# Kernel optimization log

Measured on AMD Instinct MI355X. Metric: run time of the kernel, lower is better.

The kernel has to match this reference:

```python
import jax, jax.numpy as jnp
import numpy as np

DIM = 512
HID = 1024        # dim * expansion_factor
QK = 128          # query_key_dim
G = 256           # group_size
EPS = 1e-5


def setup_inputs() -> dict:
    key = jax.random.key(0)
    ks = jax.random.split(key, 6)
    x = jax.random.normal(ks[0], (4, 4096, DIM), jnp.float32)
    ln_w = jnp.ones((DIM,), jnp.float32)
    ln_b = jnp.zeros((DIM,), jnp.float32)
    Wh = 0.02 * jax.random.normal(ks[1], (DIM, 2 * HID), jnp.float32)
    bh = jnp.zeros((2 * HID,), jnp.float32)
    Wqk = 0.02 * jax.random.normal(ks[2], (DIM, QK), jnp.float32)
    bqk = jnp.zeros((QK,), jnp.float32)
    gamma = 0.02 * jax.random.normal(ks[3], (4, QK), jnp.float32)  # nn.init.normal_(gamma, std=0.02)
    beta = jnp.zeros((4, QK), jnp.float32)
    Wo = 0.02 * jax.random.normal(ks[4], (HID, DIM), jnp.float32)
    bo = jnp.zeros((DIM,), jnp.float32)
    return {"x": x, "ln_w": ln_w, "ln_b": ln_b, "Wh": Wh, "bh": bh,
            "Wqk": Wqk, "bqk": bqk, "gamma": gamma, "beta": beta,
            "Wo": Wo, "bo": bo}


def reference(x, ln_w, ln_b, Wh, bh, Wqk, bqk, gamma, beta, Wo, bo):
    b, n, _ = x.shape
    g = n // G  # number of groups (n chosen as multiple of G -> no padding)

    # LayerNorm (torch uses biased variance)
    mu = jnp.mean(x, axis=-1, keepdims=True)
    var = jnp.mean((x - mu) ** 2, axis=-1, keepdims=True)
    normed = (x - mu) * jax.lax.rsqrt(var + EPS) * ln_w + ln_b

    # to_hidden: Linear -> SiLU, split into v / gate
    h = jax.nn.silu(normed @ Wh + bh)            # [b, n, 2*HID]
    v, gate = jnp.split(h, 2, axis=-1)           # each [b, n, HID]

    # to_qk: Linear -> SiLU, then 4-head offset/scale
    qk = jax.nn.silu(normed @ Wqk + bqk)         # [b, n, QK]
    qkh = qk[..., None, :] * gamma + beta        # [b, n, 4, QK]
    quad_q, lin_q, quad_k, lin_k = (qkh[..., i, :] for i in range(4))

    # group: b (g n) d -> b g n d
    grp = lambda t: t.reshape(b, g, G, t.shape[-1])
    qq, qk_, lq, lk, vv = map(grp, (quad_q, quad_k, lin_q, lin_k, v))

    # quadratic (group-local) attention with ReLU^2 scores, causal within group
    sim = jnp.einsum('bgid,bgjd->bgij', qq, qk_) / G
    attn = jnp.square(jnp.maximum(sim, 0.0))
    causal_mask = jnp.triu(jnp.ones((G, G), dtype=bool), 1)
    attn = jnp.where(causal_mask, 0.0, attn)
    quad_out = jnp.einsum('bgij,bgje->bgie', attn, vv)   # [b, g, G, HID]

    # linear attention across groups: per-group kv, exclusive cumsum over group dim
    lin_kv = jnp.einsum('bgnd,bgne->bgde', lk, vv) / G   # [b, g, QK, HID]
    lin_kv = jnp.cumsum(lin_kv, axis=1)
    lin_kv = jnp.pad(lin_kv, ((0, 0), (1, 0), (0, 0), (0, 0)))[:, :-1]
    lin_out = jnp.einsum('bgde,bgnd->bgne', lin_kv, lq)  # [b, g, G, HID]

    out = gate * (quad_out.reshape(b, n, HID) + lin_out.reshape(b, n, HID))
    return out @ Wo + bo + x
```

## Files before the change

kernel.cpp:

```cpp
#include <hip/hip_runtime.h>
#include <hip/hip_bf16.h>
#include <math.h>


#define BATCH 4
#define SEQ   4096
#define TROWS 16384
#define DIMD  512
#define HIDD  1024
#define QKD   128
#define GRP   256
#define NGRP  16
#define BGRP  64
#define EPIW  132
#define EPB   130

typedef unsigned short bfraw;
typedef __attribute__((ext_vector_type(8))) short bf16x8;
typedef __attribute__((ext_vector_type(8))) unsigned short u16x8;
typedef __attribute__((ext_vector_type(4))) unsigned int u32x4;
typedef __attribute__((ext_vector_type(4))) float f32x4;

__device__ __forceinline__ float bf2f(bfraw u) {
    union { float f; unsigned int i; } c;
    c.i = ((unsigned int)u) << 16;
    return c.f;
}
__device__ __forceinline__ bfraw f2bf(float f) {
    unsigned int x = __float_as_uint(f);
    unsigned int r = (x + 0x7fffu + ((x >> 16) & 1u)) >> 16;
    return (bfraw)r;
}
__device__ __forceinline__ unsigned int pkbf(float lo, float hi) {
    __hip_bfloat162 h2 = __float22bfloat162_rn(make_float2(lo, hi));
    union { __hip_bfloat162 h; unsigned int u; } c; c.h = h2;
    return c.u;
}
__device__ __forceinline__ void store16bf(bfraw* dst, const float* src) {
    u32x4 a, b;
    #pragma unroll
    for (int k = 0; k < 4; ++k) a[k] = pkbf(src[2 * k], src[2 * k + 1]);
    #pragma unroll
    for (int k = 0; k < 4; ++k) b[k] = pkbf(src[8 + 2 * k], src[8 + 2 * k + 1]);
    *(u32x4*)dst = a;
    *(u32x4*)(dst + 8) = b;
}
__device__ __forceinline__ float silu_f(float z) {
    return z / (1.f + __expf(-z));
}
__device__ __forceinline__ void gload_lds16(const void* g, void* l) {
    __builtin_amdgcn_global_load_lds(
        (const __attribute__((address_space(1))) unsigned int*)g,
        (__attribute__((address_space(3))) unsigned int*)l, 16, 0, 0);
}

__device__ __forceinline__ void mfma_step(const bfraw* As, const bfraw* Bs,
                                          f32x4 acc[4][4], int wm, int wn,
                                          int q, int mi) {
    bf16x8 af[4], bfg[4];
    #pragma unroll
    for (int i = 0; i < 4; ++i)
        af[i] = *(const bf16x8*)&As[(size_t)(wm * 64 + i * 16 + mi) * 32 + q * 8];
    #pragma unroll
    for (int j = 0; j < 4; ++j)
        bfg[j] = *(const bf16x8*)&Bs[(size_t)(wn * 64 + j * 16 + mi) * 32 + q * 8];
    #pragma unroll
    for (int i = 0; i < 4; ++i)
        #pragma unroll
        for (int j = 0; j < 4; ++j)
            acc[i][j] = __builtin_amdgcn_mfma_f32_16x16x32_bf16(af[i], bfg[j], acc[i][j], 0, 0, 0);
}

#define SMEMP_DECL                                              \
    __shared__ __align__(16) char smem_[33280];                 \
    bfraw* A0buf = (bfraw*)smem_;                               \
    bfraw* B0buf = (bfraw*)(smem_ + 8192);                      \
    bfraw* A1buf = (bfraw*)(smem_ + 16384);                     \
    bfraw* B1buf = (bfraw*)(smem_ + 24576);

#define PIPE_DSTS                                               \
    bfraw* a0d  = A0buf + wid * 512;                            \
    bfraw* a0d2 = A0buf + 2048 + wid * 512;                     \
    bfraw* b0d  = B0buf + wid * 512;                            \
    bfraw* b0d2 = B0buf + 2048 + wid * 512;                     \
    bfraw* a1d  = A1buf + wid * 512;                            \
    bfraw* a1d2 = A1buf + 2048 + wid * 512;                     \
    bfraw* b1d  = B1buf + wid * 512;                            \
    bfraw* b1d2 = B1buf + 2048 + wid * 512;

#define KLOOP_PRE(Abase, Astr, Bbase, Bstr)                                    \
    const bfraw* pa0 = (Abase) + (size_t)(t >> 2) * (Astr) + (t & 3) * 8;      \
    const bfraw* pa1 = pa0 + (size_t)64 * (Astr);                              \
    const bfraw* pb0 = (Bbase) + (size_t)(t >> 2) * (Bstr) + (t & 3) * 8;      \
    const bfraw* pb1 = pb0 + (size_t)64 * (Bstr);

#define STAGE0                                                                 \
    do { gload_lds16(pa0, a0d); gload_lds16(pa1, a0d2);                        \
         gload_lds16(pb0, b0d); gload_lds16(pb1, b0d2);                        \
         pa0 += 32; pa1 += 32; pb0 += 32; pb1 += 32; } while (0)
#define STAGE1                                                                 \
    do { gload_lds16(pa0, a1d); gload_lds16(pa1, a1d2);                        \
         gload_lds16(pb0, b1d); gload_lds16(pb1, b1d2);                        \
         pa0 += 32; pa1 += 32; pb0 += 32; pb1 += 32; } while (0)

#define PIPE_LOOP(NIT, Abase, Astr, Bbase, Bstr)                               \
    {                                                                          \
        KLOOP_PRE(Abase, Astr, Bbase, Bstr)                                    \
        STAGE0;                                                                \
        for (int it = 0; it < (NIT); it += 2) {                                \
            __syncthreads();                                                   \
            if (it + 1 < (NIT)) STAGE1;                                        \
            mfma_step(A0buf, B0buf, acc, wm, wn, q, mi);                       \
            __syncthreads();                                                   \
            if (it + 2 < (NIT)) STAGE0;                                        \
            if (it + 1 < (NIT))                                                \
                mfma_step(A1buf, B1buf, acc, wm, wn, q, mi);                   \
        }                                                                      \
        __syncthreads();                                                       \
    }

__device__ __forceinline__ int epi_row(int p, int lr) {
    return (lr < 16) ? (p * 16 + lr) : (64 + p * 16 + (lr - 16));
}

__global__ __launch_bounds__(256) void prep_kernel(const float* __restrict__ x,
                                                   const float* __restrict__ lnw,
                                                   const float* __restrict__ lnb,
                                                   const float* __restrict__ Wh,
                                                   const float* __restrict__ Wo,
                                                   const float* __restrict__ Wqk,
                                                   bfraw* __restrict__ normb,
                                                   bfraw* __restrict__ WhT,
                                                   bfraw* __restrict__ WoT,
                                                   bfraw* __restrict__ WqkT) {
    __shared__ float tile[32][33];
    int bid = blockIdx.x;
    int t = threadIdx.x;
    if (bid < 4096) {
        int row  = bid * 4 + (t >> 6);
        int lane = t & 63;
        const float* xr = x + (size_t)row * DIMD;
        float4 v0 = ((const float4*)xr)[lane];
        float4 v1 = ((const float4*)xr)[lane + 64];
        float s  = v0.x + v0.y + v0.z + v0.w + v1.x + v1.y + v1.z + v1.w;
        float ss = v0.x*v0.x + v0.y*v0.y + v0.z*v0.z + v0.w*v0.w
                 + v1.x*v1.x + v1.y*v1.y + v1.z*v1.z + v1.w*v1.w;
        #pragma unroll
        for (int off = 32; off; off >>= 1) {
            s  += __shfl_xor(s, off);
            ss += __shfl_xor(ss, off);
        }
        float mu  = s * (1.f / DIMD);
        float var = ss * (1.f / DIMD) - mu * mu;
        float inv = rsqrtf(var + 1e-5f);
        float4 w0 = ((const float4*)lnw)[lane],  w1 = ((const float4*)lnw)[lane + 64];
        float4 b0 = ((const float4*)lnb)[lane],  b1 = ((const float4*)lnb)[lane + 64];
        unsigned int o0 = pkbf((v0.x - mu) * inv * w0.x + b0.x,
                               (v0.y - mu) * inv * w0.y + b0.y);
        unsigned int o1 = pkbf((v0.z - mu) * inv * w0.z + b0.z,
                               (v0.w - mu) * inv * w0.w + b0.w);
        unsigned int o2 = pkbf((v1.x - mu) * inv * w1.x + b1.x,
                               (v1.y - mu) * inv * w1.y + b1.y);
        unsigned int o3 = pkbf((v1.z - mu) * inv * w1.z + b1.z,
                               (v1.w - mu) * inv * w1.w + b1.w);
        unsigned int* brow = (unsigned int*)(normb + (size_t)row * DIMD);
        ((uint2*)brow)[lane]      = make_uint2(o0, o1);
        ((uint2*)brow)[lane + 64] = make_uint2(o2, o3);
        return;
    }
    bid -= 4096;
    const float* in; bfraw* outp; int R, C, nx;
    if (bid < 1024)      { in = Wh;  outp = WhT;  R = DIMD; C = 2 * HIDD; nx = 64; }
    else if (bid < 1536) { bid -= 1024; in = Wo;  outp = WoT;  R = HIDD; C = DIMD; nx = 16; }
    else                 { bid -= 1536; in = Wqk; outp = WqkT; R = DIMD; C = QKD;  nx = 4; }
    int c0 = (bid % nx) * 32, r0 = (bid / nx) * 32;
    int tr = t >> 3, tc4 = (t & 7) * 4;
    float4 v = *(const float4*)&in[(size_t)(r0 + tr) * C + c0 + tc4];
    tile[tr][tc4 + 0] = v.x; tile[tr][tc4 + 1] = v.y;
    tile[tr][tc4 + 2] = v.z; tile[tr][tc4 + 3] = v.w;
    __syncthreads();
    ushort4 s;
    s.x = f2bf(tile[tc4 + 0][tr]);
    s.y = f2bf(tile[tc4 + 1][tr]);
    s.z = f2bf(tile[tc4 + 2][tr]);
    s.w = f2bf(tile[tc4 + 3][tr]);
    *(ushort4*)&outp[(size_t)(c0 + tr) * R + r0 + tc4] = s;
}

__global__ __launch_bounds__(1024, 4) void gemm_h256(
    const bfraw* __restrict__ A,
    const bfraw* __restrict__ WhT,
    const bfraw* __restrict__ WqkT,
    const float* __restrict__ bh,
    const float* __restrict__ bqk,
    const float* __restrict__ gamma,
    const float* __restrict__ beta,
    bfraw* __restrict__ vT,
    bfraw* __restrict__ gate,
    bfraw* __restrict__ qq,
    bfraw* __restrict__ lq,
    bfraw* __restrict__ kk,
    bfraw* __restrict__ lkT) {
    __shared__ __align__(16) char smem_[131072];
    const int t = threadIdx.x;
    const int lane = t & 63, wid = t >> 6;
    const int wm = wid >> 2, wn = wid & 3;
    const int q = lane >> 4, mi = lane & 15;
    int nid = (blockIdx.x & 7) * 72 + (blockIdx.x >> 3);
    const int ct = nid % 9, by = nid / 9;
    const int r0 = by * 256, c0 = ct * 256;

    const int lslot = (t & 7) ^ ((t >> 3) & 7);
    const int srow  = 2 * (t >> 3) + (lslot >> 2);
    const int skel  = (lslot & 3) * 8;
    const bfraw* Asrc = A + (size_t)(r0 + srow) * DIMD + skel;
    const bfraw* Bsrc;
    if (ct < 8) {
        Bsrc = WhT + (size_t)(c0 + srow) * DIMD + skel;
    } else {
        Bsrc = WqkT + (size_t)(srow & 127) * DIMD + skel;
    }
    const int swz = ((((mi & 1) << 2) | q) ^ ((mi >> 1) & 7)) << 4;
    const int a_off = (wm * 32 + (mi >> 1)) * 128 + swz;
    const int b_off = (wn * 32 + (mi >> 1)) * 128 + swz;

#define GH_STAGE(KT, SLOT)                                                    \
    do {                                                                      \
        char* sb_ = smem_ + (SLOT) * 32768;                                   \
        gload_lds16(Asrc + (KT) * 32, sb_ + t * 16);                          \
        gload_lds16(Bsrc + (KT) * 32, sb_ + 16384 + t * 16);                  \
    } while (0)

    f32x4 acc[4][4] = {};
    GH_STAGE(0, 0);
    GH_STAGE(1, 1);
    GH_STAGE(2, 2);
    asm volatile("s_waitcnt vmcnt(4)" ::: "memory");
    __builtin_amdgcn_s_barrier();

    #pragma unroll
    for (int j = 0; j < 16; ++j) {
        const char* cb = smem_ + (j & 3) * 32768;
        bf16x8 af[4], bfr[4];
        #pragma unroll
        for (int mf = 0; mf < 4; ++mf)
            af[mf] = *(const bf16x8*)(cb + a_off + mf * 1024);
        #pragma unroll
        for (int nf = 0; nf < 4; ++nf)
            bfr[nf] = *(const bf16x8*)(cb + 16384 + b_off + nf * 1024);
        if (j + 3 < 16) GH_STAGE(j + 3, (j + 3) & 3);
        __builtin_amdgcn_s_setprio(1);
        #pragma unroll
        for (int mf = 0; mf < 4; ++mf)
            #pragma unroll
            for (int nf = 0; nf < 4; ++nf)
                acc[mf][nf] = __builtin_amdgcn_mfma_f32_16x16x32_bf16(
                    af[mf], bfr[nf], acc[mf][nf], 0, 0, 0);
        __builtin_amdgcn_s_setprio(0);
        if (j + 3 < 16)      asm volatile("s_waitcnt vmcnt(4)" ::: "memory");
        else if (j + 2 < 16) asm volatile("s_waitcnt vmcnt(2)" ::: "memory");
        else if (j + 1 < 16) asm volatile("s_waitcnt vmcnt(0)" ::: "memory");
        __builtin_amdgcn_s_barrier();
    }
#undef GH_STAGE

    float* epi = (float*)smem_;
    if (ct == 8) {
        float* gbl = (float*)(smem_ + 67584);
        if (t < 512) { gbl[t] = gamma[t]; gbl[t + 512] = beta[t]; }
        float bq4[4];
        #pragma unroll
        for (int nf = 0; nf < 4; ++nf)
            bq4[nf] = (wn < 2) ? bqk[wn * 64 + nf * 16 + mi] : 0.f;
        #pragma unroll
        for (int p = 0; p < 4; ++p) {
            if (wm == p && wn < 2) {
                #pragma unroll
                for (int mf = 0; mf < 4; ++mf)
                    #pragma unroll
                    for (int nf = 0; nf < 4; ++nf)
                        #pragma unroll
                        for (int rg = 0; rg < 4; ++rg)
                            epi[(mf * 16 + q * 4 + rg) * 132 + wn * 64 + nf * 16 + mi] =
                                silu_f(acc[mf][nf][rg] + bq4[nf]);
            }
            __syncthreads();
            if (t < 512) {
                int lr = t >> 3, cs = (t & 7) * 16;
                float z[16];
                #pragma unroll
                for (int k = 0; k < 16; ++k) z[k] = epi[lr * 132 + cs + k];
                size_t growr = (size_t)(r0 + p * 64 + lr) * QKD + cs;
                #pragma unroll
                for (int hd = 0; hd < 3; ++hd) {
                    bfraw* arr = (hd == 0) ? qq : (hd == 1) ? lq : kk;
                    float tmp[16];
                    #pragma unroll
                    for (int k = 0; k < 16; ++k)
                        tmp[k] = z[k] * gbl[hd * 128 + cs + k] + gbl[512 + hd * 128 + cs + k];
                    store16bf(arr + growr, tmp);
                }
            } else {
                int tt = t - 512;
                int c = tt >> 2, jh = (tt & 3) * 16;
                float g3 = gbl[384 + c], e3 = gbl[896 + c];
                float tmp[16];
                #pragma unroll
                for (int k = 0; k < 16; ++k)
                    tmp[k] = epi[(jh + k) * 132 + c] * g3 + e3;
                store16bf(lkT + ((size_t)by * QKD + c) * GRP + p * 64 + jh, tmp);
            }
            __syncthreads();
        }
        return;
    }
    float bias4[4];
    #pragma unroll
    for (int nf = 0; nf < 4; ++nf)
        bias4[nf] = bh[c0 + wn * 64 + nf * 16 + mi];
    if (ct < 4) {
        #pragma unroll
        for (int p = 0; p < 4; ++p) {
            if (wm == p) {
                #pragma unroll
                for (int mf = 0; mf < 4; ++mf)
                    #pragma unroll
                    for (int nf = 0; nf < 4; ++nf)
                        #pragma unroll
                        for (int rg = 0; rg < 4; ++rg)
                            epi[(mf * 16 + q * 4 + rg) * 257 + wn * 64 + nf * 16 + mi] =
                                silu_f(acc[mf][nf][rg] + bias4[nf]);
            }
            __syncthreads();
            int e2 = t >> 2, js = (t & 3) * 16;
            float tmp[16];
            #pragma unroll
            for (int k = 0; k < 16; ++k)
                tmp[k] = epi[(js + k) * 257 + e2];
            store16bf(vT + ((size_t)by * HIDD + c0 + e2) * GRP + p * 64 + js, tmp);
            __syncthreads();
        }
    } else {
        #pragma unroll
        for (int p = 0; p < 4; ++p) {
            if (wm == p) {
                #pragma unroll
                for (int mf = 0; mf < 4; ++mf)
                    #pragma unroll
                    for (int nf = 0; nf < 4; ++nf)
                        #pragma unroll
                        for (int rg = 0; rg < 4; ++rg)
                            epi[(mf * 16 + q * 4 + rg) * 260 + wn * 64 + nf * 16 + mi] =
                                silu_f(acc[mf][nf][rg] + bias4[nf]);
            }
            __syncthreads();
            int lr = t >> 4, cs = (t & 15) * 16;
            float tmp[16];
            #pragma unroll
            for (int k = 0; k < 16; ++k)
                tmp[k] = epi[lr * 260 + cs + k];
            store16bf(gate + (size_t)(r0 + p * 64 + lr) * HIDD + (c0 - HIDD) + cs, tmp);
            __syncthreads();
        }
    }
}

__global__ __launch_bounds__(256) void simkv_kernel(const bfraw* __restrict__ qq,
                                                    const bfraw* __restrict__ kk,
                                                    bfraw* __restrict__ attn,
                                                    const bfraw* __restrict__ vT,
                                                    const bfraw* __restrict__ lkT,
                                                    bfraw* __restrict__ kvT_raw) {
    SMEMP_DECL
    float* epi = (float*)smem_;
    int t = threadIdx.x;
    int lane = t & 63, wid = t >> 6;
    int wm = wid >> 1, wn = wid & 1;
    int q = lane >> 4, mi = lane & 15;
    int bid = blockIdx.x;
    f32x4 acc[4][4] = {};
    PIPE_DSTS
    if (bid < 512) {
        int bg = bid >> 3;
        int row0 = (bid & 7) * 128;
        PIPE_LOOP(8, vT + (size_t)bg * HIDD * GRP + (size_t)row0 * GRP, GRP,
                  lkT + (size_t)bg * QKD * GRP, GRP)
        bfraw* outg = kvT_raw + (size_t)bg * HIDD * QKD;
        #pragma unroll
        for (int p = 0; p < 4; ++p) {
            #pragma unroll
            for (int j = 0; j < 4; ++j)
                #pragma unroll
                for (int rg = 0; rg < 4; ++rg)
                    epi[(wm * 16 + q * 4 + rg) * EPIW + wn * 64 + j * 16 + mi] = acc[p][j][rg];
            __syncthreads();
            int lr = t >> 3, c0t = (t & 7) * 16;
            int gr = row0 + epi_row(p, lr);
            store16bf(outg + (size_t)gr * QKD + c0t, &epi[lr * EPIW + c0t]);
            __syncthreads();
        }
        return;
    }
    int i = bid - 512;
    int bg = i & 63;
    int tid = i >> 6;
    int ry = (tid == 0) ? 0 : 1;
    int rx = (tid == 2) ? 1 : 0;
    int row0 = ry * 128, col0 = rx * 128;
    PIPE_LOOP(4, qq + (size_t)(bg * GRP + row0) * QKD, QKD,
              kk + (size_t)(bg * GRP + col0) * QKD, QKD)
    bfraw* ag = attn + (size_t)bg * GRP * GRP;
    #pragma unroll
    for (int p = 0; p < 4; ++p) {
        #pragma unroll
        for (int j = 0; j < 4; ++j) {
            int colg = col0 + wn * 64 + j * 16 + mi;
            #pragma unroll
            for (int rg = 0; rg < 4; ++rg) {
                int rowg = row0 + wm * 64 + p * 16 + q * 4 + rg;
                float s = acc[p][j][rg] * (1.f / GRP);
                s = fmaxf(s, 0.f);
                s = s * s;
                epi[(wm * 16 + q * 4 + rg) * EPIW + wn * 64 + j * 16 + mi] =
                    (colg > rowg) ? 0.f : s;
            }
        }
        __syncthreads();
        int lr = t >> 3, c0t = (t & 7) * 16;
        int gr = row0 + epi_row(p, lr);
        store16bf(ag + (size_t)gr * GRP + col0 + c0t, &epi[lr * EPIW + c0t]);
        __syncthreads();
    }
}

__global__ __launch_bounds__(256) void cumsum2_kernel(const bfraw* __restrict__ raw,
                                                      bfraw* __restrict__ ex) {
    int idx = blockIdx.x * 256 + threadIdx.x;
    int b = idx >> 17;
    int r = idx & 131071;
    const bfraw* rp = raw + (size_t)b * NGRP * 131072 + r;
    bfraw* ep = ex + (size_t)b * NGRP * 131072 + r;
    float run = 0.f;
    #pragma unroll
    for (int g = 0; g < NGRP; ++g) {
        ep[(size_t)g * 131072] = f2bf(run);
        run += bf2f(rp[(size_t)g * 131072]) * (1.f / GRP);
    }
}

__global__ __launch_bounds__(256) void quadlin_mfma(const bfraw* __restrict__ attn,
                                                    const bfraw* __restrict__ vT,
                                                    const bfraw* __restrict__ lq,
                                                    const bfraw* __restrict__ kvT_ex,
                                                    const bfraw* __restrict__ gate,
                                                    bfraw* __restrict__ gated) {
    int bg = blockIdx.z;
    int row0 = blockIdx.y * 128;
    int col0 = blockIdx.x * 128;
    SMEMP_DECL
    float* epi = (float*)smem_;
    int t = threadIdx.x;
    int lane = t & 63, wid = t >> 6;
    int wm = wid >> 1, wn = wid & 1;
    int q = lane >> 4, mi = lane & 15;
    f32x4 acc[4][4] = {};
    PIPE_DSTS
    {
        int nit = (row0 + 128) >> 5;
        PIPE_LOOP(nit, attn + (size_t)bg * GRP * GRP + (size_t)row0 * GRP, GRP,
                  vT + (size_t)bg * HIDD * GRP + (size_t)col0 * GRP, GRP)
    }
    PIPE_LOOP(4, lq + (size_t)(bg * GRP + row0) * QKD, QKD,
              kvT_ex + (size_t)bg * HIDD * QKD + (size_t)col0 * QKD, QKD)
    #pragma unroll
    for (int p = 0; p < 4; ++p) {
        #pragma unroll
        for (int j = 0; j < 4; ++j)
            #pragma unroll
            for (int rg = 0; rg < 4; ++rg)
                epi[(wm * 16 + q * 4 + rg) * EPIW + wn * 64 + j * 16 + mi] = acc[p][j][rg];
        __syncthreads();
        int lr = t >> 3, c0t = (t & 7) * 16;
        int gr = row0 + epi_row(p, lr);
        size_t grow = (size_t)bg * GRP + gr;
        const float* src = &epi[lr * EPIW + c0t];
        const bfraw* gsrc = gate + grow * HIDD + col0 + c0t;
        u16x8 g0 = *(const u16x8*)gsrc;
        u16x8 g1 = *(const u16x8*)(gsrc + 8);
        float tmp[16];
        #pragma unroll
        for (int k = 0; k < 8; ++k) tmp[k] = src[k] * bf2f(g0[k]);
        #pragma unroll
        for (int k = 0; k < 8; ++k) tmp[8 + k] = src[8 + k] * bf2f(g1[k]);
        store16bf(gated + grow * HIDD + col0 + c0t, tmp);
        __syncthreads();
    }
}

__global__ __launch_bounds__(256) void gemm_final(const bfraw* __restrict__ A,
                                                  const bfraw* __restrict__ BT,
                                                  const float* __restrict__ bo,
                                                  const float* __restrict__ x,
                                                  float* __restrict__ out) {
    SMEMP_DECL
    float* epi = (float*)smem_;
    int t = threadIdx.x;
    int lane = t & 63, wid = t >> 6;
    int wm = wid >> 1, wn = wid & 1;
    int q = lane >> 4, mi = lane & 15;
    int row0 = blockIdx.y * 128, col0 = blockIdx.x * 128;
    f32x4 acc[4][4] = {};
    PIPE_DSTS
    PIPE_LOOP(32, A + (size_t)row0 * HIDD, HIDD, BT + (size_t)col0 * HIDD, HIDD)
    #pragma unroll
    for (int p = 0; p < 4; ++p) {
        #pragma unroll
        for (int j = 0; j < 4; ++j) {
            float bv = bo[col0 + wn * 64 + j * 16 + mi];
            #pragma unroll
            for (int rg = 0; rg < 4; ++rg)
                epi[(wm * 16 + q * 4 + rg) * EPIW + wn * 64 + j * 16 + mi] =
                    acc[p][j][rg] + bv;
        }
        __syncthreads();
        int lr = t >> 3, c0t = (t & 7) * 16;
        int gr = row0 + epi_row(p, lr);
        const float* src = &epi[lr * EPIW + c0t];
        const float* xsrc = x + (size_t)gr * DIMD + col0 + c0t;
        float* dst = out + (size_t)gr * DIMD + col0 + c0t;
        #pragma unroll
        for (int v = 0; v < 4; ++v) {
            float4 a = ((const float4*)src)[v];
            float4 xv = ((const float4*)xsrc)[v];
            a.x += xv.x; a.y += xv.y; a.z += xv.z; a.w += xv.w;
            ((float4*)dst)[v] = a;
        }
        __syncthreads();
    }
}

extern "C" void kernel_launch(void* const* d_in, const int* in_sizes, int n_in,
                              void* d_out, int out_size, void* d_ws, size_t ws_size,
                              hipStream_t stream) {
    const float* x     = (const float*)d_in[0];
    const float* ln_w  = (const float*)d_in[1];
    const float* ln_b  = (const float*)d_in[2];
    const float* Wh    = (const float*)d_in[3];
    const float* bh    = (const float*)d_in[4];
    const float* Wqk   = (const float*)d_in[5];
    const float* bqk   = (const float*)d_in[6];
    const float* gamma = (const float*)d_in[7];
    const float* beta  = (const float*)d_in[8];
    const float* Wo    = (const float*)d_in[9];
    const float* bo    = (const float*)d_in[10];
    float* out = (float*)d_out;

    char* outb_ = (char*)d_out;
    bfraw* attn = (bfraw*)(outb_);
    bfraw* qq   = (bfraw*)(outb_ + 8388608);
    bfraw* kk   = (bfraw*)(outb_ + 12582912);
    bfraw* lq   = (bfraw*)(outb_ + 16777216);
    bfraw* WhT  = (bfraw*)(outb_ + 20971520);
    bfraw* WqkT = (bfraw*)(outb_ + 23068672);

    char* wsb = (char*)d_ws;
    bfraw* vT      = (bfraw*)(wsb);
    bfraw* gate    = (bfraw*)(wsb + 33554432);
    bfraw* gated   = (bfraw*)(wsb + 67108864);
    bfraw* normb   = (bfraw*)(wsb + 100663296);
    bfraw* kvT_raw = (bfraw*)(wsb + 117440512);
    bfraw* kvT_ex  = (bfraw*)(wsb + 134217728);
    bfraw* lkT     = (bfraw*)(wsb + 150994944);
    bfraw* WoT     = (bfraw*)(wsb + 155189248);

    prep_kernel<<<4096 + 1024 + 512 + 64, 256, 0, stream>>>(
        x, ln_w, ln_b, Wh, Wo, Wqk, normb, WhT, WoT, WqkT);
    gemm_h256<<<576, 1024, 0, stream>>>(
        normb, WhT, WqkT, bh, bqk, gamma, beta, vT, gate, qq, lq, kk, lkT);
    simkv_kernel<<<512 + 192, 256, 0, stream>>>(qq, kk, attn, vT, lkT, kvT_raw);
    cumsum2_kernel<<<(BATCH * QKD * HIDD) / 256, 256, 0, stream>>>(kvT_raw, kvT_ex);
    quadlin_mfma<<<dim3(HIDD / 128, GRP / 128, BGRP), 256, 0, stream>>>(
        attn, vT, lq, kvT_ex, gate, gated);
    gemm_final<<<dim3(DIMD / 128, TROWS / 128), 256, 0, stream>>>(gated, WoT, bo, x, out);
}
```

Baseline: 272.9 us.

## Rewrite final projection GEMM with 256x128 tiles, 1024 threads and triple-buffered LDS

The output projection GEMM moves from 128x128 tiles on 256-thread blocks to 256x128 tiles on 1024-thread blocks, with a 3-stage asynchronous global-to-LDS pipeline, XOR-swizzled LDS layout and MFMA priority hints. Block indices are remapped so neighbouring blocks share A row tiles, and the grid becomes 256 blocks. The goal is more reuse per tile and better overlap of loads with MFMA work on this GEMM. In exchange each block uses 144KB of LDS, so only one block fits per CU, and the epilogue is serialized across four wave-row passes.

```diff
diff --git a/kernel.cpp b/kernel.cpp
--- a/kernel.cpp
+++ b/kernel.cpp
@@ -497,41 +497,103 @@
     }
 }
 
-__global__ __launch_bounds__(256) void gemm_final(const bfraw* __restrict__ A,
-                                                  const bfraw* __restrict__ BT,
-                                                  const float* __restrict__ bo,
-                                                  const float* __restrict__ x,
-                                                  float* __restrict__ out) {
-    SMEMP_DECL
+__global__ __launch_bounds__(1024, 4) void gemm_final(
+    const bfraw* __restrict__ A,
+    const bfraw* __restrict__ BT,
+    const float* __restrict__ bo,
+    const float* __restrict__ x,
+    float* __restrict__ out) {
+    __shared__ __align__(16) char smem_[147456];
+    const int t = threadIdx.x;
+    const int lane = t & 63, wid = t >> 6;
+    const int wm = wid >> 2, wn = wid & 3;
+    const int q = lane >> 4, mi = lane & 15;
+    int nid = (blockIdx.x & 7) * 32 + (blockIdx.x >> 3);
+    const int by = nid >> 2, cx = nid & 3;
+    const int r0 = by * 256, c0 = cx * 128;
+
+    const int lslot = (t & 7) ^ ((t >> 3) & 7);
+    const int a_row = 2 * (t >> 3) + (lslot >> 2);
+    const int a_kel = (lslot & 3) * 8;
+    const bfraw* Asrc = A + (size_t)(r0 + a_row) * HIDD + a_kel;
+    const int u = t & 511;
+    const int lsb = (u & 7) ^ ((u >> 3) & 7);
+    const int b_row = 2 * (u >> 3) + (lsb >> 2);
+    const int b_kel = (lsb & 3) * 8 + (t >> 9) * 32;
+    const bfraw* Bsrc = BT + (size_t)(c0 + b_row) * HIDD + b_kel;
+
+    const int swz = ((((mi & 1) << 2) | q) ^ ((mi >> 1) & 7)) << 4;
+    const int a_off = (wm * 32 + (mi >> 1)) * 128 + swz;
+    const int b_off = (wn * 16 + (mi >> 1)) * 128 + swz;
+
+#define GF_STAGE(SS, SLOT)                                                    \
+    do {                                                                      \
+        char* sb_ = smem_ + (SLOT) * 49152;                                   \
+        gload_lds16(Asrc + (SS) * 64,      sb_ + t * 16);                     \
+        gload_lds16(Asrc + (SS) * 64 + 32, sb_ + 16384 + t * 16);             \
+        gload_lds16(Bsrc + (SS) * 64,      sb_ + 32768 + t * 16);             \
+    } while (0)
+
+    f32x4 acc[4][2] = {};
+    GF_STAGE(0, 0);
+    GF_STAGE(1, 1);
+    asm volatile("s_waitcnt vmcnt(3)" ::: "memory");
+    __builtin_amdgcn_s_barrier();
+
+    #pragma unroll
+    for (int ss = 0; ss < 16; ++ss) {
+        if (ss + 2 < 16) GF_STAGE(ss + 2, (ss + 2) % 3);
+        const char* cb = smem_ + (ss % 3) * 49152;
+        #pragma unroll
+        for (int h = 0; h < 2; ++h) {
+            bf16x8 af[4], bfr[2];
+            #pragma unroll
+            for (int mf = 0; mf < 4; ++mf)
+                af[mf] = *(const bf16x8*)(cb + h * 16384 + a_off + mf * 1024);
+            #pragma unroll
+            for (int nf = 0; nf < 2; ++nf)
+                bfr[nf] = *(const bf16x8*)(cb + 32768 + h * 8192 + b_off + nf * 1024);
+            __builtin_amdgcn_s_setprio(1);
+            #pragma unroll
+            for (int mf = 0; mf < 4; ++mf)
+                #pragma unroll
+                for (int nf = 0; nf < 2; ++nf)
+                    acc[mf][nf] = __builtin_amdgcn_mfma_f32_16x16x32_bf16(
+                        af[mf], bfr[nf], acc[mf][nf], 0, 0, 0);
+            __builtin_amdgcn_s_setprio(0);
+        }
+        if (ss + 2 < 16)      asm volatile("s_waitcnt vmcnt(3)" ::: "memory");
+        else if (ss + 1 < 16) asm volatile("s_waitcnt vmcnt(0)" ::: "memory");
+        __builtin_amdgcn_s_barrier();
+    }
+#undef GF_STAGE
+
     float* epi = (float*)smem_;
-    int t = threadIdx.x;
-    int lane = t & 63, wid = t >> 6;
-    int wm = wid >> 1, wn = wid & 1;
-    int q = lane >> 4, mi = lane & 15;
-    int row0 = blockIdx.y * 128, col0 = blockIdx.x * 128;
-    f32x4 acc[4][4] = {};
-    PIPE_DSTS
-    PIPE_LOOP(32, A + (size_t)row0 * HIDD, HIDD, BT + (size_t)col0 * HIDD, HIDD)
+    float bo2[2];
+    #pragma unroll
+    for (int nf = 0; nf < 2; ++nf)
+        bo2[nf] = bo[c0 + wn * 32 + nf * 16 + mi];
     #pragma unroll
     for (int p = 0; p < 4; ++p) {
-        #pragma unroll
-        for (int j = 0; j < 4; ++j) {
-            float bv = bo[col0 + wn * 64 + j * 16 + mi];
-            #pragma unroll
-            for (int rg = 0; rg < 4; ++rg)
-                epi[(wm * 16 + q * 4 + rg) * EPIW + wn * 64 + j * 16 + mi] =
-                    acc[p][j][rg] + bv;
+        if (wm == p) {
+            #pragma unroll
+            for (int mf = 0; mf < 4; ++mf)
+                #pragma unroll
+                for (int nf = 0; nf < 2; ++nf)
+                    #pragma unroll
+                    for (int rg = 0; rg < 4; ++rg)
+                        epi[(mf * 16 + q * 4 + rg) * 132 + wn * 32 + nf * 16 + mi] =
+                            acc[mf][nf][rg] + bo2[nf];
         }
         __syncthreads();
-        int lr = t >> 3, c0t = (t & 7) * 16;
-        int gr = row0 + epi_row(p, lr);
-        const float* src = &epi[lr * EPIW + c0t];
-        const float* xsrc = x + (size_t)gr * DIMD + col0 + c0t;
-        float* dst = out + (size_t)gr * DIMD + col0 + c0t;
-        #pragma unroll
-        for (int v = 0; v < 4; ++v) {
+        int lr = t >> 4, cs = (t & 15) * 8;
+        const float* src = epi + lr * 132 + cs;
+        const float* xs = x + (size_t)(r0 + p * 64 + lr) * DIMD + c0 + cs;
+        float* dst = out + (size_t)(r0 + p * 64 + lr) * DIMD + c0 + cs;
+        #pragma unroll
+        for (int v = 0; v < 2; ++v) {
             float4 a = ((const float4*)src)[v];
-            float4 xv = ((const float4*)xsrc)[v];
+            float4 xv = ((const float4*)xs)[v];
             a.x += xv.x; a.y += xv.y; a.z += xv.z; a.w += xv.w;
             ((float4*)dst)[v] = a;
         }
@@ -581,5 +643,5 @@
     cumsum2_kernel<<<(BATCH * QKD * HIDD) / 256, 256, 0, stream>>>(kvT_raw, kvT_ex);
     quadlin_mfma<<<dim3(HIDD / 128, GRP / 128, BGRP), 256, 0, stream>>>(
         attn, vT, lq, kvT_ex, gate, gated);
-    gemm_final<<<dim3(DIMD / 128, TROWS / 128), 256, 0, stream>>>(gated, WoT, bo, x, out);
-}
+    gemm_final<<<256, 1024, 0, stream>>>(gated, WoT, bo, x, out);
+}
```

Result: no change. 270.2 us (-1.0%).
